# Performance work log

Hardware: AMD Instinct MI355X
Metric: run time of the kernel (lower is better)

The kernel has to match this reference:

```python
import jax, jax.numpy as jnp
import numpy as np

N_NODES = 50000
N_EDGES = 800000
N_GRAPHS = 256
F_IN = 128
H = 64
N_CLASSES = 10


def setup_inputs() -> dict:
    key = jax.random.key(0)
    ks = jax.random.split(key, 12)
    x = jax.random.normal(ks[0], (N_NODES, F_IN), dtype=jnp.float32)
    edge_index = jax.random.randint(ks[1], (2, N_EDGES), 0, N_NODES, dtype=jnp.int64)
    batch = jnp.sort(jax.random.randint(ks[2], (N_NODES,), 0, N_GRAPHS, dtype=jnp.int64))
    def glorot(k, fan_in, fan_out):
        lim = np.sqrt(6.0 / (fan_in + fan_out)).astype(np.float32)
        return jax.random.uniform(k, (fan_in, fan_out), jnp.float32, -lim, lim)
    return {
        "x": x,
        "edge_index": edge_index,
        "batch": batch,
        "W1": glorot(ks[3], F_IN, H), "b1": jnp.zeros((H,), jnp.float32),
        "W2": glorot(ks[4], H, H),    "b2": jnp.zeros((H,), jnp.float32),
        "W3": glorot(ks[5], H, H),    "b3": jnp.zeros((H,), jnp.float32),
        "Wm": glorot(ks[6], H, N_CLASSES), "bm": jnp.zeros((N_CLASSES,), jnp.float32),
    }


def _gcn_norm(edge_index, n_nodes):
    # Add self-loops, unit edge weights, symmetric normalization (PyG gcn_norm).
    loops = jnp.arange(n_nodes, dtype=edge_index.dtype)
    row = jnp.concatenate([edge_index[0], loops])  # source
    col = jnp.concatenate([edge_index[1], loops])  # target (aggregation index)
    deg = jax.ops.segment_sum(jnp.ones_like(col, dtype=jnp.float32), col,
                              num_segments=n_nodes)
    dinv = jnp.where(deg > 0, jax.lax.rsqrt(deg), 0.0)
    norm = dinv[row] * dinv[col]  # [E + N]
    return row, col, norm


def _gcn_conv(x, row, col, norm, W, b, n_nodes):
    h = x @ W                                   # [N, H] dense transform
    msg = h[row] * norm[:, None]                # gather + scale  [E+N, H]
    out = jax.ops.segment_sum(msg, col, num_segments=n_nodes)  # scatter-add
    return out + b


def _l2_normalize(x, eps=1e-12):
    n = jnp.sqrt(jnp.sum(x * x, axis=-1, keepdims=True))
    return x / jnp.maximum(n, eps)


def reference(x, edge_index, batch, W1, b1, W2, b2, W3, b3, Wm, bm):
    n = x.shape[0]
    row, col, norm = _gcn_norm(edge_index, n)
    h = x
    for (W, b) in ((W1, b1), (W2, b2), (W3, b3)):
        h = _gcn_conv(h, row, col, norm, W, b, n)
        h = _l2_normalize(h)       # emb_normalize
        h = jax.nn.relu(h)         # gnn_non_linear
    node_emb = h
    # global_mean_pool over graphs
    sums = jax.ops.segment_sum(h, batch, num_segments=N_GRAPHS)
    counts = jax.ops.segment_sum(jnp.ones((n,), jnp.float32), batch,
                                 num_segments=N_GRAPHS)
    graph_emb = sums / jnp.maximum(counts, 1.0)[:, None]
    logits = graph_emb @ Wm + bm
    probs = jax.nn.softmax(logits, axis=-1)
    return logits, probs, node_emb, graph_emb
```

## Files before the change

### kernel.cpp

```cpp
#include <hip/hip_runtime.h>
#include <math.h>

#define HH 64
#define BSH 8
#define BSZ 256

typedef _Float16 half_t;
typedef _Float16 half4_t __attribute__((ext_vector_type(4)));


__global__ void k_init(int* __restrict__ bucket_cnt, float* __restrict__ sums,
                       int nb, int pn) {
    int i = blockIdx.x * blockDim.x + threadIdx.x;
    if (i < nb) bucket_cnt[i] = 0;
    if (i < pn) sums[i] = 0.f;
}

__global__ __launch_bounds__(256) void k_bhist(const int* __restrict__ col, int E,
                                               int* __restrict__ bucket_cnt, int nb) {
    __shared__ int h[BSZ];
    int t = threadIdx.x;
    h[t] = 0;
    __syncthreads();
    int stride = gridDim.x * blockDim.x;
    for (int e = blockIdx.x * blockDim.x + t; e < E; e += stride)
        atomicAdd(&h[col[e] >> BSH], 1);
    __syncthreads();
    if (t < nb && h[t]) atomicAdd(&bucket_cnt[t], h[t]);
}

__global__ __launch_bounds__(256) void k_bscan(const int* __restrict__ bc,
                                               int* __restrict__ base,
                                               int* __restrict__ cursor, int nb) {
    __shared__ int s[256];
    __shared__ int carry_s;
    int t = threadIdx.x;
    if (t == 0) carry_s = 0;
    __syncthreads();
    for (int off = 0; off < nb; off += 256) {
        int i = off + t;
        int v = (i < nb) ? bc[i] : 0;
        s[t] = v;
        __syncthreads();
        for (int d = 1; d < 256; d <<= 1) {
            int x = s[t];
            if (t >= d) x += s[t - d];
            __syncthreads();
            s[t] = x;
            __syncthreads();
        }
        int carry = carry_s;
        int excl = carry + s[t] - v;
        if (i < nb) { base[i] = excl; cursor[i] = excl; }
        int tot = s[255];
        __syncthreads();
        if (t == 0) carry_s = carry + tot;
        __syncthreads();
    }
    if (t == 0) base[nb] = carry_s;
}

__global__ __launch_bounds__(256) void k_bscatter(const int* __restrict__ row,
                                                  const int* __restrict__ col, int E,
                                                  int* __restrict__ gcursor,
                                                  int* __restrict__ pair, int nb) {
    __shared__ int h[BSZ];
    __shared__ int cur[BSZ];
    int t = threadIdx.x;
    h[t] = 0;
    __syncthreads();
    int stride = gridDim.x * blockDim.x;
    for (int e = blockIdx.x * blockDim.x + t; e < E; e += stride)
        atomicAdd(&h[col[e] >> BSH], 1);
    __syncthreads();
    {
        int c = h[t];
        cur[t] = (t < nb && c > 0) ? atomicAdd(&gcursor[t], c) : 0;
    }
    __syncthreads();
    for (int e = blockIdx.x * blockDim.x + t; e < E; e += stride) {
        int c = col[e];
        int pos = atomicAdd(&cur[c >> BSH], 1);
        pair[pos] = (row[e] & 0xFFFF) | ((c & (BSZ - 1)) << 16);
    }
}

__global__ __launch_bounds__(256) void k_bcsr(const int* __restrict__ pair,
                                              const int* __restrict__ base,
                                              int* __restrict__ rowptr,
                                              int* __restrict__ cnt,
                                              float* __restrict__ dinv,
                                              int* __restrict__ csr, int n) {
    __shared__ int lcnt[BSZ];
    __shared__ int ssc[BSZ];
    __shared__ int lcur[BSZ];
    const int b = blockIdx.x;
    const int t = threadIdx.x;
    const int nd0 = b << BSH;
    const int e0 = base[b];
    const int e1 = base[b + 1];

    lcnt[t] = 0;
    __syncthreads();
    for (int e = e0 + t; e < e1; e += 256)
        atomicAdd(&lcnt[(pair[e] >> 16) & (BSZ - 1)], 1);
    __syncthreads();
    int v = lcnt[t];
    ssc[t] = v;
    __syncthreads();
    for (int d = 1; d < 256; d <<= 1) {
        int x = ssc[t];
        if (t >= d) x += ssc[t - d];
        __syncthreads();
        ssc[t] = x;
        __syncthreads();
    }
    int excl = ssc[t] - v;
    lcur[t] = e0 + excl;
    int node = nd0 + t;
    if (node < n) {
        rowptr[node] = e0 + excl;
        cnt[node]    = v;
        dinv[node]   = rsqrtf((float)(v + 1));
    }
    __syncthreads();
    for (int e = e0 + t; e < e1; e += 256) {
        int p = pair[e];
        int pos = atomicAdd(&lcur[(p >> 16) & (BSZ - 1)], 1);
        csr[pos] = p & 0xFFFF;
    }
}

template<int FIN, bool SCALE, bool HIN, bool HOUT>
__global__ __launch_bounds__(256, (FIN == 128) ? 3 : 4)
void k_gemm(const void* __restrict__ xin, const float* __restrict__ W,
            const float* __restrict__ dinv, void* __restrict__ out, int n) {
    constexpr int KC = 32;
    constexpr int XS = 68;
    __shared__ __align__(16) float Ws[FIN][HH];
    __shared__ __align__(16) float xs_t[KC][XS];
    const int tid = threadIdx.x;
    const int tx = tid & 15;
    const int ty = tid >> 4;
    const int node0 = blockIdx.x * 64;
    if (node0 >= n) return;

    for (int i = tid * 4; i < FIN * HH; i += 1024)
        *(float4*)&Ws[0][i] = *(const float4*)&W[i];

    float acc[4][4] = {};
    const int rr0 = tid >> 3;
    const int cc  = (tid & 7) * 4;

    for (int kc = 0; kc < FIN; kc += KC) {
        __syncthreads();
        for (int rr = rr0; rr < 64; rr += 32) {
            float4 v = make_float4(0.f, 0.f, 0.f, 0.f);
            if (node0 + rr < n) {
                if constexpr (HIN) {
                    half4_t hv = *(const half4_t*)((const half_t*)xin +
                                   (size_t)(node0 + rr) * FIN + kc + cc);
                    v = make_float4((float)hv.x, (float)hv.y, (float)hv.z, (float)hv.w);
                } else {
                    v = *(const float4*)((const float*)xin +
                                   (size_t)(node0 + rr) * FIN + kc + cc);
                }
            }
            xs_t[cc + 0][rr] = v.x;
            xs_t[cc + 1][rr] = v.y;
            xs_t[cc + 2][rr] = v.z;
            xs_t[cc + 3][rr] = v.w;
        }
        __syncthreads();
#pragma unroll 4
        for (int k = 0; k < KC; ++k) {
            float4 a4 = *(const float4*)&xs_t[k][ty * 4];
            float4 b4 = *(const float4*)&Ws[kc + k][tx * 4];
            acc[0][0] = fmaf(a4.x, b4.x, acc[0][0]);
            acc[0][1] = fmaf(a4.x, b4.y, acc[0][1]);
            acc[0][2] = fmaf(a4.x, b4.z, acc[0][2]);
            acc[0][3] = fmaf(a4.x, b4.w, acc[0][3]);
            acc[1][0] = fmaf(a4.y, b4.x, acc[1][0]);
            acc[1][1] = fmaf(a4.y, b4.y, acc[1][1]);
            acc[1][2] = fmaf(a4.y, b4.z, acc[1][2]);
            acc[1][3] = fmaf(a4.y, b4.w, acc[1][3]);
            acc[2][0] = fmaf(a4.z, b4.x, acc[2][0]);
            acc[2][1] = fmaf(a4.z, b4.y, acc[2][1]);
            acc[2][2] = fmaf(a4.z, b4.z, acc[2][2]);
            acc[2][3] = fmaf(a4.z, b4.w, acc[2][3]);
            acc[3][0] = fmaf(a4.w, b4.x, acc[3][0]);
            acc[3][1] = fmaf(a4.w, b4.y, acc[3][1]);
            acc[3][2] = fmaf(a4.w, b4.z, acc[3][2]);
            acc[3][3] = fmaf(a4.w, b4.w, acc[3][3]);
        }
    }

#pragma unroll
    for (int i = 0; i < 4; ++i) {
        int node = node0 + ty * 4 + i;
        if (node < n) {
            float d = SCALE ? dinv[node] : 1.f;
            float r0 = acc[i][0] * d, r1 = acc[i][1] * d;
            float r2 = acc[i][2] * d, r3 = acc[i][3] * d;
            if constexpr (HOUT) {
                half4_t o = {(half_t)r0, (half_t)r1, (half_t)r2, (half_t)r3};
                *(half4_t*)((half_t*)out + (size_t)node * HH + tx * 4) = o;
            } else {
                *(float4*)((float*)out + (size_t)node * HH + tx * 4) =
                    make_float4(r0, r1, r2, r3);
            }
        }
    }
}

template<bool WEIGHTED, bool HOUT>
__global__ __launch_bounds__(256) void k_gather_q(const half_t* __restrict__ lin,
                                                  const int* __restrict__ csr,
                                                  const int* __restrict__ rowptr,
                                                  const int* __restrict__ cnt,
                                                  const float* __restrict__ dinv,
                                                  const float* __restrict__ b,
                                                  void* __restrict__ hout, int n) {
    int node = blockIdx.x * 4 + (threadIdx.x >> 6);
    int lane = threadIdx.x & 63;
    if (node >= n) return;
    const int q  = lane >> 4;
    const int fl = (lane & 15) * 4;
    int start = rowptr[node];
    int end = start + cnt[node];
    float di = dinv[node];

    float4 a0 = make_float4(0.f, 0.f, 0.f, 0.f);
    float4 a1 = make_float4(0.f, 0.f, 0.f, 0.f);

    for (int base = start; base < end; base += 64) {
        int m = end - base; if (m > 64) m = 64;
        int idx = base + lane;
        int   sv = (idx < end) ? csr[idx] : 0;
        float wv;
        if (WEIGHTED) wv = (idx < end) ? dinv[sv] : 0.f;
        else          wv = (idx < end) ? 1.f : 0.f;
        for (int j = 0; j < m; j += 16) {
            int l = j + q * 4;
            int   s0 = __shfl(sv, l, 64);
            int   s1 = __shfl(sv, l + 1, 64);
            int   s2 = __shfl(sv, l + 2, 64);
            int   s3 = __shfl(sv, l + 3, 64);
            float w0 = __shfl(wv, l, 64);
            float w1 = __shfl(wv, l + 1, 64);
            float w2 = __shfl(wv, l + 2, 64);
            float w3 = __shfl(wv, l + 3, 64);
            half4_t v0 = *(const half4_t*)&lin[(size_t)s0 * HH + fl];
            half4_t v1 = *(const half4_t*)&lin[(size_t)s1 * HH + fl];
            half4_t v2 = *(const half4_t*)&lin[(size_t)s2 * HH + fl];
            half4_t v3 = *(const half4_t*)&lin[(size_t)s3 * HH + fl];
            a0.x = fmaf(w0, (float)v0.x, a0.x); a0.y = fmaf(w0, (float)v0.y, a0.y);
            a0.z = fmaf(w0, (float)v0.z, a0.z); a0.w = fmaf(w0, (float)v0.w, a0.w);
            a1.x = fmaf(w1, (float)v1.x, a1.x); a1.y = fmaf(w1, (float)v1.y, a1.y);
            a1.z = fmaf(w1, (float)v1.z, a1.z); a1.w = fmaf(w1, (float)v1.w, a1.w);
            a0.x = fmaf(w2, (float)v2.x, a0.x); a0.y = fmaf(w2, (float)v2.y, a0.y);
            a0.z = fmaf(w2, (float)v2.z, a0.z); a0.w = fmaf(w2, (float)v2.w, a0.w);
            a1.x = fmaf(w3, (float)v3.x, a1.x); a1.y = fmaf(w3, (float)v3.y, a1.y);
            a1.z = fmaf(w3, (float)v3.z, a1.z); a1.w = fmaf(w3, (float)v3.w, a1.w);
        }
    }
    float4 acc = make_float4(a0.x + a1.x, a0.y + a1.y, a0.z + a1.z, a0.w + a1.w);
#pragma unroll
    for (int off = 16; off < 64; off <<= 1) {
        acc.x += __shfl_xor(acc.x, off, 64);
        acc.y += __shfl_xor(acc.y, off, 64);
        acc.z += __shfl_xor(acc.z, off, 64);
        acc.w += __shfl_xor(acc.w, off, 64);
    }
    half4_t self = *(const half4_t*)&lin[(size_t)node * HH + fl];
    float sw = WEIGHTED ? di : 1.f;
    acc.x = fmaf(sw, (float)self.x, acc.x);
    acc.y = fmaf(sw, (float)self.y, acc.y);
    acc.z = fmaf(sw, (float)self.z, acc.z);
    acc.w = fmaf(sw, (float)self.w, acc.w);
    float4 b4 = *(const float4*)&b[fl];
    float4 v4 = make_float4(fmaf(di, acc.x, b4.x), fmaf(di, acc.y, b4.y),
                            fmaf(di, acc.z, b4.z), fmaf(di, acc.w, b4.w));
    float ss = v4.x * v4.x + v4.y * v4.y + v4.z * v4.z + v4.w * v4.w;
#pragma unroll
    for (int off = 1; off < 16; off <<= 1) ss += __shfl_xor(ss, off, 64);
    float inv = 1.f / fmaxf(sqrtf(ss), 1e-12f);
    v4.x = fmaxf(v4.x * inv, 0.f);
    v4.y = fmaxf(v4.y * inv, 0.f);
    v4.z = fmaxf(v4.z * inv, 0.f);
    v4.w = fmaxf(v4.w * inv, 0.f);
    if (q == 0) {
        if constexpr (HOUT) {
            half4_t o = {(half_t)v4.x, (half_t)v4.y, (half_t)v4.z, (half_t)v4.w};
            *(half4_t*)((half_t*)hout + (size_t)node * HH + fl) = o;
        } else {
            *(float4*)((float*)hout + (size_t)node * HH + fl) = v4;
        }
    }
}

__global__ __launch_bounds__(256) void k_pool(const float* __restrict__ node_emb,
                                              const int* __restrict__ batch,
                                              float* __restrict__ sums,
                                              float* __restrict__ cnts, int n) {
    const int NPW = 16;
    int wave = blockIdx.x * 4 + (threadIdx.x >> 6);
    int lane = threadIdx.x & 63;
    int start = wave * NPW;
    if (start >= n) return;
    int end = start + NPW; if (end > n) end = n;
    int cur = batch[start];
    float acc = 0.f;
    int runlen = 0;
    for (int node = start; node < end; ++node) {
        int g = batch[node];
        if (g != cur) {
            atomicAdd(&sums[(size_t)cur * HH + lane], acc);
            if (lane == 0) atomicAdd(&cnts[cur], (float)runlen);
            acc = 0.f; runlen = 0; cur = g;
        }
        acc += node_emb[(size_t)node * HH + lane];
        ++runlen;
    }
    atomicAdd(&sums[(size_t)cur * HH + lane], acc);
    if (lane == 0) atomicAdd(&cnts[cur], (float)runlen);
}

__global__ void k_final2(const float* __restrict__ sums, const float* __restrict__ cnts,
                         const float* __restrict__ Wm, const float* __restrict__ bm,
                         float* __restrict__ logits, float* __restrict__ probs,
                         float* __restrict__ graph_emb) {
    int g = blockIdx.x;
    int lane = threadIdx.x;
    float mean = sums[(size_t)g * HH + lane] / fmaxf(cnts[g], 1.0f);
    graph_emb[(size_t)g * HH + lane] = mean;

    __shared__ float semb[HH];
    __shared__ float slog[16];
    semb[lane] = mean;
    __syncthreads();
    if (lane < 10) {
        float acc = bm[lane];
        for (int k = 0; k < HH; ++k) acc = fmaf(semb[k], Wm[k * 10 + lane], acc);
        slog[lane] = acc;
    }
    __syncthreads();
    if (lane < 10) {
        float mx = -1e30f;
        for (int j = 0; j < 10; ++j) mx = fmaxf(mx, slog[j]);
        float den = 0.f;
        for (int j = 0; j < 10; ++j) den += __expf(slog[j] - mx);
        float lg = slog[lane];
        logits[g * 10 + lane] = lg;
        probs[g * 10 + lane] = __expf(lg - mx) / den;
    }
}


extern "C" void kernel_launch(void* const* d_in, const int* in_sizes, int n_in,
                              void* d_out, int out_size, void* d_ws, size_t ws_size,
                              hipStream_t stream) {
    const float* x     = (const float*)d_in[0];
    const int*   ei    = (const int*)  d_in[1];
    const int*   batch = (const int*)  d_in[2];
    const float* W1 = (const float*)d_in[3];  const float* b1 = (const float*)d_in[4];
    const float* W2 = (const float*)d_in[5];  const float* b2 = (const float*)d_in[6];
    const float* W3 = (const float*)d_in[7];  const float* b3 = (const float*)d_in[8];
    const float* Wm = (const float*)d_in[9];  const float* bm = (const float*)d_in[10];

    const int N = in_sizes[2];
    const int E = in_sizes[1] / 2;
    const int G = (out_size - N * HH) / (2 * 10 + HH);
    const int NB = (N + BSZ - 1) >> BSH;

    const int* row = ei;
    const int* col = ei + E;

    float* out       = (float*)d_out;
    float* logits    = out;
    float* probs     = out + (size_t)G * 10;
    float* node_emb  = out + (size_t)2 * G * 10;
    float* graph_emb = node_emb + (size_t)N * HH;

    char* w = (char*)d_ws;
    auto alloc = [&](size_t bytes) { char* p = w; w += (bytes + 255) & ~(size_t)255; return p; };
    float* dinv    = (float*)alloc((size_t)N * 4);
    int*   cnt     = (int*)  alloc((size_t)N * 4);
    int*   rowptr  = (int*)  alloc((size_t)N * 4);
    int*   bucket_cnt    = (int*)alloc((size_t)(NB + 1) * 4);
    int*   bucket_base   = (int*)alloc((size_t)(NB + 1) * 4);
    int*   bucket_cursor = (int*)alloc((size_t)(NB + 1) * 4);
    float* sums    = (float*)alloc((size_t)G * HH * 4 + (size_t)G * 4);
    float* cnts    = sums + (size_t)G * HH;
    int*   pairbuf = (int*)  alloc((size_t)E * 4);
    int*   csr     = (int*)  alloc((size_t)E * 4);
    half_t* bufA   = (half_t*)alloc((size_t)N * HH * 2);
    half_t* bufB   = (half_t*)alloc((size_t)N * HH * 2);

    const int B = 256;
    dim3 blk(B);
    int node_blocks = (N + 3) / 4;
    int gemm_blocks = (N + 63) / 64;
    int poolN = G * HH + G;
    int initB = (poolN + B - 1) / B;
    int pool_blocks = (N + 63) / 64;

    k_init<<<initB, blk, 0, stream>>>(bucket_cnt, sums, NB, poolN);
    k_bhist<<<256, blk, 0, stream>>>(col, E, bucket_cnt, NB);
    k_bscan<<<1, blk, 0, stream>>>(bucket_cnt, bucket_base, bucket_cursor, NB);
    k_bscatter<<<256, blk, 0, stream>>>(row, col, E, bucket_cursor, pairbuf, NB);
    k_bcsr<<<NB, blk, 0, stream>>>(pairbuf, bucket_base, rowptr, cnt, dinv, csr, N);

    k_gemm<128, false, false, true><<<gemm_blocks, blk, 0, stream>>>(x, W1, dinv, bufA, N);
    k_gather_q<true, true><<<node_blocks, blk, 0, stream>>>(bufA, csr, rowptr, cnt, dinv, b1, bufB, N);
    k_gemm<64, true, true, true><<<gemm_blocks, blk, 0, stream>>>(bufB, W2, dinv, bufA, N);
    k_gather_q<false, true><<<node_blocks, blk, 0, stream>>>(bufA, csr, rowptr, cnt, dinv, b2, bufB, N);
    k_gemm<64, true, true, true><<<gemm_blocks, blk, 0, stream>>>(bufB, W3, dinv, bufA, N);
    k_gather_q<false, false><<<node_blocks, blk, 0, stream>>>(bufA, csr, rowptr, cnt, dinv, b3, node_emb, N);

    k_pool<<<pool_blocks, blk, 0, stream>>>(node_emb, batch, sums, cnts, N);
    k_final2<<<G, dim3(64), 0, stream>>>(sums, cnts, Wm, bm, logits, probs, graph_emb);
}
```

Measured before the change: 266.4 us.

## Fuse edge histogram into first GEMM, merge scan into scatter, fuse pool with final

The bucket histogram is computed per block inside the first GEMM kernel and written as per-block partial counts. The scatter kernel then derives global and per-block offsets itself, which removes the init, global histogram and single-block scan launches. Pooling now uses a binary search over the sorted batch array, one block per graph, with the softmax head in the same kernel, so no atomics or zero-init are needed. In exchange, every scatter block redundantly reads all 256 partial histograms, and the pooling relies on batch being sorted.

```diff
diff --git a/kernel.cpp b/kernel.cpp
--- a/kernel.cpp
+++ b/kernel.cpp
@@ -4,145 +4,36 @@
 #define HH 64
 #define BSH 8
 #define BSZ 256
+#define HBLK 256
+#define HSTRIDE (HBLK * 256)
 
 typedef _Float16 half_t;
 typedef _Float16 half4_t __attribute__((ext_vector_type(4)));
 
-
-__global__ void k_init(int* __restrict__ bucket_cnt, float* __restrict__ sums,
-                       int nb, int pn) {
-    int i = blockIdx.x * blockDim.x + threadIdx.x;
-    if (i < nb) bucket_cnt[i] = 0;
-    if (i < pn) sums[i] = 0.f;
-}
-
-__global__ __launch_bounds__(256) void k_bhist(const int* __restrict__ col, int E,
-                                               int* __restrict__ bucket_cnt, int nb) {
-    __shared__ int h[BSZ];
-    int t = threadIdx.x;
-    h[t] = 0;
-    __syncthreads();
-    int stride = gridDim.x * blockDim.x;
-    for (int e = blockIdx.x * blockDim.x + t; e < E; e += stride)
-        atomicAdd(&h[col[e] >> BSH], 1);
-    __syncthreads();
-    if (t < nb && h[t]) atomicAdd(&bucket_cnt[t], h[t]);
-}
-
-__global__ __launch_bounds__(256) void k_bscan(const int* __restrict__ bc,
-                                               int* __restrict__ base,
-                                               int* __restrict__ cursor, int nb) {
-    __shared__ int s[256];
-    __shared__ int carry_s;
-    int t = threadIdx.x;
-    if (t == 0) carry_s = 0;
-    __syncthreads();
-    for (int off = 0; off < nb; off += 256) {
-        int i = off + t;
-        int v = (i < nb) ? bc[i] : 0;
-        s[t] = v;
-        __syncthreads();
-        for (int d = 1; d < 256; d <<= 1) {
-            int x = s[t];
-            if (t >= d) x += s[t - d];
-            __syncthreads();
-            s[t] = x;
-            __syncthreads();
-        }
-        int carry = carry_s;
-        int excl = carry + s[t] - v;
-        if (i < nb) { base[i] = excl; cursor[i] = excl; }
-        int tot = s[255];
-        __syncthreads();
-        if (t == 0) carry_s = carry + tot;
-        __syncthreads();
-    }
-    if (t == 0) base[nb] = carry_s;
-}
-
-__global__ __launch_bounds__(256) void k_bscatter(const int* __restrict__ row,
-                                                  const int* __restrict__ col, int E,
-                                                  int* __restrict__ gcursor,
-                                                  int* __restrict__ pair, int nb) {
-    __shared__ int h[BSZ];
-    __shared__ int cur[BSZ];
-    int t = threadIdx.x;
-    h[t] = 0;
-    __syncthreads();
-    int stride = gridDim.x * blockDim.x;
-    for (int e = blockIdx.x * blockDim.x + t; e < E; e += stride)
-        atomicAdd(&h[col[e] >> BSH], 1);
-    __syncthreads();
-    {
-        int c = h[t];
-        cur[t] = (t < nb && c > 0) ? atomicAdd(&gcursor[t], c) : 0;
-    }
-    __syncthreads();
-    for (int e = blockIdx.x * blockDim.x + t; e < E; e += stride) {
-        int c = col[e];
-        int pos = atomicAdd(&cur[c >> BSH], 1);
-        pair[pos] = (row[e] & 0xFFFF) | ((c & (BSZ - 1)) << 16);
-    }
-}
-
-__global__ __launch_bounds__(256) void k_bcsr(const int* __restrict__ pair,
-                                              const int* __restrict__ base,
-                                              int* __restrict__ rowptr,
-                                              int* __restrict__ cnt,
-                                              float* __restrict__ dinv,
-                                              int* __restrict__ csr, int n) {
-    __shared__ int lcnt[BSZ];
-    __shared__ int ssc[BSZ];
-    __shared__ int lcur[BSZ];
-    const int b = blockIdx.x;
-    const int t = threadIdx.x;
-    const int nd0 = b << BSH;
-    const int e0 = base[b];
-    const int e1 = base[b + 1];
-
-    lcnt[t] = 0;
-    __syncthreads();
-    for (int e = e0 + t; e < e1; e += 256)
-        atomicAdd(&lcnt[(pair[e] >> 16) & (BSZ - 1)], 1);
-    __syncthreads();
-    int v = lcnt[t];
-    ssc[t] = v;
-    __syncthreads();
-    for (int d = 1; d < 256; d <<= 1) {
-        int x = ssc[t];
-        if (t >= d) x += ssc[t - d];
-        __syncthreads();
-        ssc[t] = x;
-        __syncthreads();
-    }
-    int excl = ssc[t] - v;
-    lcur[t] = e0 + excl;
-    int node = nd0 + t;
-    if (node < n) {
-        rowptr[node] = e0 + excl;
-        cnt[node]    = v;
-        dinv[node]   = rsqrtf((float)(v + 1));
-    }
-    __syncthreads();
-    for (int e = e0 + t; e < e1; e += 256) {
-        int p = pair[e];
-        int pos = atomicAdd(&lcur[(p >> 16) & (BSZ - 1)], 1);
-        csr[pos] = p & 0xFFFF;
-    }
-}
-
-template<int FIN, bool SCALE, bool HIN, bool HOUT>
-__global__ __launch_bounds__(256, (FIN == 128) ? 3 : 4)
-void k_gemm(const void* __restrict__ xin, const float* __restrict__ W,
-            const float* __restrict__ dinv, void* __restrict__ out, int n) {
+__global__ __launch_bounds__(256, 3)
+void k_gemm1_hist(const float* __restrict__ x, const float* __restrict__ W,
+                  half_t* __restrict__ out, int n,
+                  const int* __restrict__ col, int E, int* __restrict__ ph) {
+    constexpr int FIN = 128;
     constexpr int KC = 32;
-    constexpr int XS = 68;
     __shared__ __align__(16) float Ws[FIN][HH];
-    __shared__ __align__(16) float xs_t[KC][XS];
+    __shared__ __align__(16) float xs_t[KC][68];
+    __shared__ int hh[BSZ];
     const int tid = threadIdx.x;
+    const int bid = blockIdx.x;
+
+    if (bid < HBLK) {
+        hh[tid] = 0;
+        __syncthreads();
+        for (int e = bid * 256 + tid; e < E; e += HSTRIDE)
+            atomicAdd(&hh[col[e] >> BSH], 1);
+        __syncthreads();
+        ph[bid * BSZ + tid] = hh[tid];
+    }
+
     const int tx = tid & 15;
     const int ty = tid >> 4;
-    const int node0 = blockIdx.x * 64;
+    const int node0 = bid * 64;
     if (node0 >= n) return;
 
     for (int i = tid * 4; i < FIN * HH; i += 1024)
@@ -156,16 +47,7 @@
         __syncthreads();
         for (int rr = rr0; rr < 64; rr += 32) {
             float4 v = make_float4(0.f, 0.f, 0.f, 0.f);
-            if (node0 + rr < n) {
-                if constexpr (HIN) {
-                    half4_t hv = *(const half4_t*)((const half_t*)xin +
-                                   (size_t)(node0 + rr) * FIN + kc + cc);
-                    v = make_float4((float)hv.x, (float)hv.y, (float)hv.z, (float)hv.w);
-                } else {
-                    v = *(const float4*)((const float*)xin +
-                                   (size_t)(node0 + rr) * FIN + kc + cc);
-                }
-            }
+            if (node0 + rr < n) v = *(const float4*)&x[(size_t)(node0 + rr) * FIN + kc + cc];
             xs_t[cc + 0][rr] = v.x;
             xs_t[cc + 1][rr] = v.y;
             xs_t[cc + 2][rr] = v.z;
@@ -194,21 +76,165 @@
             acc[3][3] = fmaf(a4.w, b4.w, acc[3][3]);
         }
     }
-
 #pragma unroll
     for (int i = 0; i < 4; ++i) {
         int node = node0 + ty * 4 + i;
         if (node < n) {
-            float d = SCALE ? dinv[node] : 1.f;
-            float r0 = acc[i][0] * d, r1 = acc[i][1] * d;
-            float r2 = acc[i][2] * d, r3 = acc[i][3] * d;
-            if constexpr (HOUT) {
-                half4_t o = {(half_t)r0, (half_t)r1, (half_t)r2, (half_t)r3};
-                *(half4_t*)((half_t*)out + (size_t)node * HH + tx * 4) = o;
-            } else {
-                *(float4*)((float*)out + (size_t)node * HH + tx * 4) =
-                    make_float4(r0, r1, r2, r3);
+            half4_t o = {(half_t)acc[i][0], (half_t)acc[i][1],
+                         (half_t)acc[i][2], (half_t)acc[i][3]};
+            *(half4_t*)(out + (size_t)node * HH + tx * 4) = o;
+        }
+    }
+}
+
+__global__ __launch_bounds__(256) void k_bscatter2(const int* __restrict__ row,
+                                                   const int* __restrict__ col, int E,
+                                                   const int* __restrict__ ph,
+                                                   int* __restrict__ base,
+                                                   int* __restrict__ pair, int nb) {
+    __shared__ int cur[BSZ];
+    __shared__ int ssc[BSZ];
+    const int b = blockIdx.x;
+    const int t = threadIdx.x;
+    int before = 0, total = 0;
+    for (int k = 0; k < HBLK; ++k) {
+        int v = ph[k * BSZ + t];
+        total += v;
+        if (k < b) before += v;
+    }
+    ssc[t] = total;
+    __syncthreads();
+    for (int d = 1; d < 256; d <<= 1) {
+        int x2 = ssc[t];
+        if (t >= d) x2 += ssc[t - d];
+        __syncthreads();
+        ssc[t] = x2;
+        __syncthreads();
+    }
+    int excl = ssc[t] - total;
+    cur[t] = excl + before;
+    if (b == 0) {
+        if (t < nb) base[t] = excl;
+        if (t == 0) base[nb] = E;
+    }
+    __syncthreads();
+    for (int e = b * 256 + t; e < E; e += HSTRIDE) {
+        int c = col[e];
+        int pos = atomicAdd(&cur[c >> BSH], 1);
+        pair[pos] = (row[e] & 0xFFFF) | ((c & (BSZ - 1)) << 16);
+    }
+}
+
+__global__ __launch_bounds__(256) void k_bcsr(const int* __restrict__ pair,
+                                              const int* __restrict__ base,
+                                              int* __restrict__ rowptr,
+                                              int* __restrict__ cnt,
+                                              float* __restrict__ dinv,
+                                              int* __restrict__ csr, int n) {
+    __shared__ int lcnt[BSZ];
+    __shared__ int ssc[BSZ];
+    __shared__ int lcur[BSZ];
+    const int b = blockIdx.x;
+    const int t = threadIdx.x;
+    const int nd0 = b << BSH;
+    const int e0 = base[b];
+    const int e1 = base[b + 1];
+
+    lcnt[t] = 0;
+    __syncthreads();
+    for (int e = e0 + t; e < e1; e += 256)
+        atomicAdd(&lcnt[(pair[e] >> 16) & (BSZ - 1)], 1);
+    __syncthreads();
+    int v = lcnt[t];
+    ssc[t] = v;
+    __syncthreads();
+    for (int d = 1; d < 256; d <<= 1) {
+        int x2 = ssc[t];
+        if (t >= d) x2 += ssc[t - d];
+        __syncthreads();
+        ssc[t] = x2;
+        __syncthreads();
+    }
+    int excl = ssc[t] - v;
+    lcur[t] = e0 + excl;
+    int node = nd0 + t;
+    if (node < n) {
+        rowptr[node] = e0 + excl;
+        cnt[node]    = v;
+        dinv[node]   = rsqrtf((float)(v + 1));
+    }
+    __syncthreads();
+    for (int e = e0 + t; e < e1; e += 256) {
+        int pr = pair[e];
+        int pos = atomicAdd(&lcur[(pr >> 16) & (BSZ - 1)], 1);
+        csr[pos] = pr & 0xFFFF;
+    }
+}
+
+template<int FIN>
+__global__ __launch_bounds__(256, 4)
+void k_gemm(const half_t* __restrict__ xin, const float* __restrict__ W,
+            const float* __restrict__ dinv, half_t* __restrict__ out, int n) {
+    constexpr int KC = 32;
+    __shared__ __align__(16) float Ws[FIN][HH];
+    __shared__ __align__(16) float xs_t[KC][68];
+    const int tid = threadIdx.x;
+    const int tx = tid & 15;
+    const int ty = tid >> 4;
+    const int node0 = blockIdx.x * 64;
+    if (node0 >= n) return;
+
+    for (int i = tid * 4; i < FIN * HH; i += 1024)
+        *(float4*)&Ws[0][i] = *(const float4*)&W[i];
+
+    float acc[4][4] = {};
+    const int rr0 = tid >> 3;
+    const int cc  = (tid & 7) * 4;
+
+    for (int kc = 0; kc < FIN; kc += KC) {
+        __syncthreads();
+        for (int rr = rr0; rr < 64; rr += 32) {
+            float4 v = make_float4(0.f, 0.f, 0.f, 0.f);
+            if (node0 + rr < n) {
+                half4_t hv = *(const half4_t*)(xin + (size_t)(node0 + rr) * FIN + kc + cc);
+                v = make_float4((float)hv.x, (float)hv.y, (float)hv.z, (float)hv.w);
             }
+            xs_t[cc + 0][rr] = v.x;
+            xs_t[cc + 1][rr] = v.y;
+            xs_t[cc + 2][rr] = v.z;
+            xs_t[cc + 3][rr] = v.w;
+        }
+        __syncthreads();
+#pragma unroll 4
+        for (int k = 0; k < KC; ++k) {
+            float4 a4 = *(const float4*)&xs_t[k][ty * 4];
+            float4 b4 = *(const float4*)&Ws[kc + k][tx * 4];
+            acc[0][0] = fmaf(a4.x, b4.x, acc[0][0]);
+            acc[0][1] = fmaf(a4.x, b4.y, acc[0][1]);
+            acc[0][2] = fmaf(a4.x, b4.z, acc[0][2]);
+            acc[0][3] = fmaf(a4.x, b4.w, acc[0][3]);
+            acc[1][0] = fmaf(a4.y, b4.x, acc[1][0]);
+            acc[1][1] = fmaf(a4.y, b4.y, acc[1][1]);
+            acc[1][2] = fmaf(a4.y, b4.z, acc[1][2]);
+            acc[1][3] = fmaf(a4.y, b4.w, acc[1][3]);
+            acc[2][0] = fmaf(a4.z, b4.x, acc[2][0]);
+            acc[2][1] = fmaf(a4.z, b4.y, acc[2][1]);
+            acc[2][2] = fmaf(a4.z, b4.z, acc[2][2]);
+            acc[2][3] = fmaf(a4.z, b4.w, acc[2][3]);
+            acc[3][0] = fmaf(a4.w, b4.x, acc[3][0]);
+            acc[3][1] = fmaf(a4.w, b4.y, acc[3][1]);
+            acc[3][2] = fmaf(a4.w, b4.z, acc[3][2]);
+            acc[3][3] = fmaf(a4.w, b4.w, acc[3][3]);
+        }
+    }
+#pragma unroll
+    for (int i = 0; i < 4; ++i) {
+        int node = node0 + ty * 4 + i;
+        if (node < n) {
+            float d = dinv[node];
+            half4_t o = {(half_t)(acc[i][0] * d), (half_t)(acc[i][1] * d),
+                         (half_t)(acc[i][2] * d), (half_t)(acc[i][3] * d)};
+            *(half4_t*)(out + (size_t)node * HH + tx * 4) = o;
         }
     }
 }
@@ -299,60 +325,52 @@
     }
 }
 
-__global__ __launch_bounds__(256) void k_pool(const float* __restrict__ node_emb,
-                                              const int* __restrict__ batch,
-                                              float* __restrict__ sums,
-                                              float* __restrict__ cnts, int n) {
-    const int NPW = 16;
-    int wave = blockIdx.x * 4 + (threadIdx.x >> 6);
-    int lane = threadIdx.x & 63;
-    int start = wave * NPW;
-    if (start >= n) return;
-    int end = start + NPW; if (end > n) end = n;
-    int cur = batch[start];
-    float acc = 0.f;
-    int runlen = 0;
-    for (int node = start; node < end; ++node) {
-        int g = batch[node];
-        if (g != cur) {
-            atomicAdd(&sums[(size_t)cur * HH + lane], acc);
-            if (lane == 0) atomicAdd(&cnts[cur], (float)runlen);
-            acc = 0.f; runlen = 0; cur = g;
-        }
-        acc += node_emb[(size_t)node * HH + lane];
-        ++runlen;
-    }
-    atomicAdd(&sums[(size_t)cur * HH + lane], acc);
-    if (lane == 0) atomicAdd(&cnts[cur], (float)runlen);
-}
-
-__global__ void k_final2(const float* __restrict__ sums, const float* __restrict__ cnts,
-                         const float* __restrict__ Wm, const float* __restrict__ bm,
-                         float* __restrict__ logits, float* __restrict__ probs,
-                         float* __restrict__ graph_emb) {
-    int g = blockIdx.x;
-    int lane = threadIdx.x;
-    float mean = sums[(size_t)g * HH + lane] / fmaxf(cnts[g], 1.0f);
-    graph_emb[(size_t)g * HH + lane] = mean;
-
+__global__ __launch_bounds__(256) void k_poolfinal(const float* __restrict__ node_emb,
+                                                   const int* __restrict__ batch,
+                                                   const float* __restrict__ Wm,
+                                                   const float* __restrict__ bm,
+                                                   float* __restrict__ logits,
+                                                   float* __restrict__ probs,
+                                                   float* __restrict__ graph_emb, int n) {
+    __shared__ float part[4][HH];
     __shared__ float semb[HH];
     __shared__ float slog[16];
-    semb[lane] = mean;
-    __syncthreads();
-    if (lane < 10) {
-        float acc = bm[lane];
-        for (int k = 0; k < HH; ++k) acc = fmaf(semb[k], Wm[k * 10 + lane], acc);
-        slog[lane] = acc;
-    }
-    __syncthreads();
-    if (lane < 10) {
+    const int g = blockIdx.x;
+    const int tid = threadIdx.x;
+    const int lane = tid & 63, w = tid >> 6;
+
+    int lo = 0, hi = n;
+    while (lo < hi) { int mid = (lo + hi) >> 1; if (batch[mid] < g) lo = mid + 1; else hi = mid; }
+    const int s = lo;
+    hi = n;
+    while (lo < hi) { int mid = (lo + hi) >> 1; if (batch[mid] < g + 1) lo = mid + 1; else hi = mid; }
+    const int e2 = lo;
+
+    float acc = 0.f;
+    for (int i = s + w; i < e2; i += 4) acc += node_emb[(size_t)i * HH + lane];
+    part[w][lane] = acc;
+    __syncthreads();
+    if (tid < HH) {
+        float m = part[0][tid] + part[1][tid] + part[2][tid] + part[3][tid];
+        m /= fmaxf((float)(e2 - s), 1.f);
+        graph_emb[(size_t)g * HH + tid] = m;
+        semb[tid] = m;
+    }
+    __syncthreads();
+    if (tid < 10) {
+        float a2 = bm[tid];
+        for (int k = 0; k < HH; ++k) a2 = fmaf(semb[k], Wm[k * 10 + tid], a2);
+        slog[tid] = a2;
+    }
+    __syncthreads();
+    if (tid < 10) {
         float mx = -1e30f;
         for (int j = 0; j < 10; ++j) mx = fmaxf(mx, slog[j]);
         float den = 0.f;
         for (int j = 0; j < 10; ++j) den += __expf(slog[j] - mx);
-        float lg = slog[lane];
-        logits[g * 10 + lane] = lg;
-        probs[g * 10 + lane] = __expf(lg - mx) / den;
+        float lg = slog[tid];
+        logits[g * 10 + tid] = lg;
+        probs[g * 10 + tid] = __expf(lg - mx) / den;
     }
 }
 
@@ -387,11 +405,8 @@
     float* dinv    = (float*)alloc((size_t)N * 4);
     int*   cnt     = (int*)  alloc((size_t)N * 4);
     int*   rowptr  = (int*)  alloc((size_t)N * 4);
-    int*   bucket_cnt    = (int*)alloc((size_t)(NB + 1) * 4);
-    int*   bucket_base   = (int*)alloc((size_t)(NB + 1) * 4);
-    int*   bucket_cursor = (int*)alloc((size_t)(NB + 1) * 4);
-    float* sums    = (float*)alloc((size_t)G * HH * 4 + (size_t)G * 4);
-    float* cnts    = sums + (size_t)G * HH;
+    int*   ph      = (int*)  alloc((size_t)HBLK * BSZ * 4);
+    int*   base    = (int*)  alloc((size_t)(NB + 1) * 4);
     int*   pairbuf = (int*)  alloc((size_t)E * 4);
     int*   csr     = (int*)  alloc((size_t)E * 4);
     half_t* bufA   = (half_t*)alloc((size_t)N * HH * 2);
@@ -401,23 +416,17 @@
     dim3 blk(B);
     int node_blocks = (N + 3) / 4;
     int gemm_blocks = (N + 63) / 64;
-    int poolN = G * HH + G;
-    int initB = (poolN + B - 1) / B;
-    int pool_blocks = (N + 63) / 64;
-
-    k_init<<<initB, blk, 0, stream>>>(bucket_cnt, sums, NB, poolN);
-    k_bhist<<<256, blk, 0, stream>>>(col, E, bucket_cnt, NB);
-    k_bscan<<<1, blk, 0, stream>>>(bucket_cnt, bucket_base, bucket_cursor, NB);
-    k_bscatter<<<256, blk, 0, stream>>>(row, col, E, bucket_cursor, pairbuf, NB);
-    k_bcsr<<<NB, blk, 0, stream>>>(pairbuf, bucket_base, rowptr, cnt, dinv, csr, N);
-
-    k_gemm<128, false, false, true><<<gemm_blocks, blk, 0, stream>>>(x, W1, dinv, bufA, N);
+    int g1_blocks = gemm_blocks > HBLK ? gemm_blocks : HBLK;
+
+    k_gemm1_hist<<<g1_blocks, blk, 0, stream>>>(x, W1, bufA, N, col, E, ph);
+    k_bscatter2<<<HBLK, blk, 0, stream>>>(row, col, E, ph, base, pairbuf, NB);
+    k_bcsr<<<NB, blk, 0, stream>>>(pairbuf, base, rowptr, cnt, dinv, csr, N);
+
     k_gather_q<true, true><<<node_blocks, blk, 0, stream>>>(bufA, csr, rowptr, cnt, dinv, b1, bufB, N);
-    k_gemm<64, true, true, true><<<gemm_blocks, blk, 0, stream>>>(bufB, W2, dinv, bufA, N);
+    k_gemm<64><<<gemm_blocks, blk, 0, stream>>>(bufB, W2, dinv, bufA, N);
     k_gather_q<false, true><<<node_blocks, blk, 0, stream>>>(bufA, csr, rowptr, cnt, dinv, b2, bufB, N);
-    k_gemm<64, true, true, true><<<gemm_blocks, blk, 0, stream>>>(bufB, W3, dinv, bufA, N);
+    k_gemm<64><<<gemm_blocks, blk, 0, stream>>>(bufB, W3, dinv, bufA, N);
     k_gather_q<false, false><<<node_blocks, blk, 0, stream>>>(bufA, csr, rowptr, cnt, dinv, b3, node_emb, N);
 
-    k_pool<<<pool_blocks, blk, 0, stream>>>(node_emb, batch, sums, cnts, N);
-    k_final2<<<G, dim3(64), 0, stream>>>(sums, cnts, Wm, bm, logits, probs, graph_emb);
-}
+    k_poolfinal<<<G, blk, 0, stream>>>(node_emb, batch, Wm, bm, logits, probs, graph_emb, N);
+}
```

After: 269.9 us. About the same (+1.3%).
